# Optimization experiments

Hardware: AMD Instinct MI355X
Metric: run time of the kernel (lower is better)

## Reference

```python
import jax, jax.numpy as jnp
import numpy as np

N_NODES = 65536
N_EDGES = 262144
N_GRAPHS = 2048
NF = 16   # num_node_features
EF = 6    # num_edge_features
H1, H2, H3 = 32, 16, 8  # conv1 out, conv2 out, lin1 out


def _lin_init(key, fan_in, fan_out):
    kw, kb = jax.random.split(key)
    s = 1.0 / np.sqrt(fan_in)
    w = jax.random.uniform(kw, (fan_in, fan_out), minval=-s, maxval=s, dtype=jnp.float32)
    b = jax.random.uniform(kb, (fan_out,), minval=-s, maxval=s, dtype=jnp.float32)
    return w, b


def setup_inputs() -> dict:
    key = jax.random.key(0)
    ks = jax.random.split(key, 16)
    inp = {}
    inp["x_p"] = jax.random.normal(ks[0], (N_NODES, NF), dtype=jnp.float32)
    inp["x_d"] = jax.random.normal(ks[1], (4, NF), dtype=jnp.float32)  # unused by forward
    inp["edge_attr_p"] = jax.random.uniform(ks[2], (N_EDGES, EF), dtype=jnp.float32)
    inp["edge_attr_d"] = jax.random.uniform(ks[3], (4, EF), dtype=jnp.float32)  # unused
    inp["edge_index_p"] = jax.random.randint(ks[4], (2, N_EDGES), 0, N_NODES, dtype=jnp.int32)
    inp["x_p_batch"] = jnp.sort(jax.random.randint(ks[5], (N_NODES,), 0, N_GRAPHS, dtype=jnp.int32))
    # conv1: NNConv(NF, 32); edge nn: Linear(EF,16) -> ReLU -> Linear(16, NF*32)
    inp["nn1_w1"], inp["nn1_b1"] = _lin_init(ks[6], EF, 16)
    inp["nn1_w2"], inp["nn1_b2"] = _lin_init(ks[7], 16, NF * H1)
    inp["root1"] = _lin_init(ks[8], NF, H1)[0]
    inp["bias1"] = jnp.zeros((H1,), dtype=jnp.float32)
    # conv2: NNConv(32, 16); edge nn: Linear(EF,16) -> ReLU -> Linear(16, 32*16)
    inp["nn2_w1"], inp["nn2_b1"] = _lin_init(ks[9], EF, 16)
    inp["nn2_w2"], inp["nn2_b2"] = _lin_init(ks[10], 16, H1 * H2)
    inp["root2"] = _lin_init(ks[11], H1, H2)[0]
    inp["bias2"] = jnp.zeros((H2,), dtype=jnp.float32)
    # attention pooling gate: Linear(NF,NF) -> ReLU -> Linear(NF,1)
    inp["gate_w1"], inp["gate_b1"] = _lin_init(ks[12], NF, NF)
    inp["gate_w2"], inp["gate_b2"] = _lin_init(ks[13], NF, 1)
    # head: Linear(16+16, 8) -> Linear(8, 1)  (attention=True)
    inp["lin1_w"], inp["lin1_b"] = _lin_init(ks[14], H2 + NF, H3)
    inp["lin2_w"], inp["lin2_b"] = _lin_init(ks[15], H3, 1)
    return inp


def _nnconv(x, edge_attr, src, dst, w1, b1, w2, b2, root, bias, in_c, out_c, n_nodes):
    # per-edge dynamic weight matrix Theta(e) : [E, in_c, out_c]
    h = jax.nn.relu(edge_attr @ w1 + b1) @ w2 + b2
    w_dyn = h.reshape(-1, in_c, out_c)
    msg = jnp.einsum('ei,eio->eo', x[src], w_dyn)          # [E, out_c]
    agg = jax.ops.segment_sum(msg, dst, num_segments=n_nodes)  # scatter-add
    return agg + x @ root + bias


def _attention_pool(x, batch, gw1, gb1, gw2, gb2, n_graphs):
    g = (jax.nn.relu(x @ gw1 + gb1) @ gw2 + gb2)[:, 0]     # [N] gate logits
    m = jax.ops.segment_max(g, batch, num_segments=n_graphs)
    e = jnp.exp(g - m[batch])
    s = jax.ops.segment_sum(e, batch, num_segments=n_graphs)
    alpha = e / s[batch]                                    # per-graph softmax
    return jax.ops.segment_sum(alpha[:, None] * x, batch, num_segments=n_graphs)


def _mean_pool(x, batch, n_graphs):
    s = jax.ops.segment_sum(x, batch, num_segments=n_graphs)
    cnt = jax.ops.segment_sum(jnp.ones((x.shape[0],), x.dtype), batch, num_segments=n_graphs)
    return s / jnp.maximum(cnt, 1.0)[:, None]


def reference(x_p, x_d, edge_attr_p, edge_attr_d, edge_index_p, x_p_batch,
              nn1_w1, nn1_b1, nn1_w2, nn1_b2, root1, bias1,
              nn2_w1, nn2_b1, nn2_w2, nn2_b2, root2, bias2,
              gate_w1, gate_b1, gate_w2, gate_b2,
              lin1_w, lin1_b, lin2_w, lin2_b):
    src, dst = edge_index_p[0], edge_index_p[1]
    # attention pooling on raw node features (attention=True)
    x_att = _attention_pool(x_p, x_p_batch, gate_w1, gate_b1, gate_w2, gate_b2, N_GRAPHS)
    # two NNConv layers with ReLU
    h = jax.nn.relu(_nnconv(x_p, edge_attr_p, src, dst, nn1_w1, nn1_b1, nn1_w2, nn1_b2,
                            root1, bias1, NF, H1, N_NODES))
    h = jax.nn.relu(_nnconv(h, edge_attr_p, src, dst, nn2_w1, nn2_b1, nn2_w2, nn2_b2,
                            root2, bias2, H1, H2, N_NODES))
    g = _mean_pool(h, x_p_batch, N_GRAPHS)                  # [B, 16]
    g = jnp.concatenate([g, x_att], axis=1)                 # [B, 32]
    # dropout p=0.5 is identity in eval mode
    g = g @ lin1_w + lin1_b
    out = g @ lin2_w + lin2_b                               # [B, 1]
    return out
```

## Files before the change

### kernel.cpp

```cpp
#include <hip/hip_runtime.h>

#define NN 65536
#define NE 262144
#define NG 2048

typedef __attribute__((ext_vector_type(16))) float f32x16;
typedef __attribute__((ext_vector_type(4)))  float f32x4;
typedef __attribute__((ext_vector_type(8)))  __bf16 bf16x8;

__device__ inline unsigned pack2(float a, float b) {
    return __builtin_amdgcn_perm(__float_as_uint(b), __float_as_uint(a), 0x07060302u);
}
__device__ inline float lof(float p) {
    return p - __uint_as_float(__float_as_uint(p) & 0xffff0000u);
}
__device__ inline bf16x8 asb(uint4 u) { return __builtin_bit_cast(bf16x8, u); }

__global__ __launch_bounds__(256) void k_gate(const float* __restrict__ x,
    const float* __restrict__ gw1, const float* __restrict__ gb1,
    const float* __restrict__ gw2, const float* __restrict__ gb2,
    float* __restrict__ g_all)
{
    __shared__ float s_w[256];
    __shared__ float s_b[16];
    __shared__ float s_w2[16];
    __shared__ float s_b2;
    int tid = threadIdx.x;
    s_w[tid & 255] = gw1[tid & 255];
    if (tid < 16) { s_b[tid] = gb1[tid]; s_w2[tid] = gw2[tid]; }
    if (tid == 0) s_b2 = gb2[0];
    __syncthreads();
    int n = blockIdx.x * 256 + tid;
    if (n >= NN) return;
    float xv[16];
    const float4* xp = (const float4*)(x + (size_t)n * 16);
#pragma unroll
    for (int i = 0; i < 4; ++i) {
        float4 t = xp[i];
        xv[4*i] = t.x; xv[4*i+1] = t.y; xv[4*i+2] = t.z; xv[4*i+3] = t.w;
    }
    float g = s_b2;
#pragma unroll
    for (int j = 0; j < 16; ++j) {
        float a = s_b[j];
#pragma unroll
        for (int i = 0; i < 16; ++i) a += xv[i] * s_w[i*16 + j];
        g += fmaxf(a, 0.f) * s_w2[j];
    }
    g_all[n] = g;
}

__global__ void k_goffsets(const int* __restrict__ batch, int* __restrict__ goffs)
{
    int g = blockIdx.x * blockDim.x + threadIdx.x;
    if (g > NG) return;
    int lo = 0, hi = NN;
    while (lo < hi) {
        int mid = (lo + hi) >> 1;
        if (batch[mid] < g) lo = mid + 1; else hi = mid;
    }
    goffs[g] = lo;
}

__global__ __launch_bounds__(64) void k_attpool(const float* __restrict__ x,
    const float* __restrict__ g_all, const int* __restrict__ goffs,
    float* __restrict__ x_att)
{
    int g = blockIdx.x;
    int lane = threadIdx.x;
    int s = goffs[g], e = goffs[g + 1];
    if (s >= e) {
        if (lane < 16) x_att[g*16 + lane] = 0.f;
        return;
    }
    float m = -1e30f;
    for (int i = s + lane; i < e; i += 64) m = fmaxf(m, g_all[i]);
#pragma unroll
    for (int d = 32; d; d >>= 1) m = fmaxf(m, __shfl_xor(m, d));
    float sum = 0.f;
    for (int i = s + lane; i < e; i += 64) sum += expf(g_all[i] - m);
#pragma unroll
    for (int d = 32; d; d >>= 1) sum += __shfl_xor(sum, d);
    float inv = 1.f / sum;
    int f = lane & 15, sub = lane >> 4;
    float acc = 0.f;
    for (int i = s + sub; i < e; i += 4) {
        float w = expf(g_all[i] - m) * inv;
        acc += w * x[(size_t)i*16 + f];
    }
    acc += __shfl_xor(acc, 16);
    acc += __shfl_xor(acc, 32);
    if (lane < 16) x_att[g*16 + f] = acc;
}

__global__ __launch_bounds__(256) void k_hist(const int* __restrict__ ei, int* __restrict__ cnt)
{
    int e = blockIdx.x * 256 + threadIdx.x;
    if (e >= NE) return;
    atomicAdd(&cnt[ei[NE + e]], 1);
}

__global__ __launch_bounds__(256) void k_scan_blk(const int* __restrict__ cnt,
    int* __restrict__ offs, int* __restrict__ bsum)
{
    __shared__ int s[256];
    int t = threadIdx.x, b = blockIdx.x;
    int v = cnt[b*256 + t];
    s[t] = v;
    __syncthreads();
#pragma unroll
    for (int d = 1; d < 256; d <<= 1) {
        int add = (t >= d) ? s[t - d] : 0;
        __syncthreads();
        s[t] += add;
        __syncthreads();
    }
    offs[b*256 + t] = s[t] - v;
    if (t == 255) bsum[b] = s[255];
}

__global__ __launch_bounds__(256) void k_scan_top(const int* __restrict__ bsum,
    int* __restrict__ boff)
{
    __shared__ int s[256];
    int t = threadIdx.x;
    int v = bsum[t];
    s[t] = v;
    __syncthreads();
#pragma unroll
    for (int d = 1; d < 256; d <<= 1) {
        int add = (t >= d) ? s[t - d] : 0;
        __syncthreads();
        s[t] += add;
        __syncthreads();
    }
    boff[t] = s[t] - v;
}

__global__ __launch_bounds__(256) void k_scan_add(int* __restrict__ offs,
    const int* __restrict__ boff)
{
    int i = blockIdx.x * 256 + threadIdx.x;
    if (i == 0) offs[NN] = NE;
    if (i >= NN) return;
    offs[i] += boff[i >> 8];
}

__global__ __launch_bounds__(256) void k_scatter(const int* __restrict__ ei,
    const int* __restrict__ offs, int* __restrict__ cur, int* __restrict__ eperm)
{
    int e = blockIdx.x * 256 + threadIdx.x;
    if (e >= NE) return;
    int d = ei[NE + e];
    int pos = offs[d] + atomicAdd(&cur[d], 1);
    eperm[pos] = e;
}

__global__ __launch_bounds__(256) void k_prep(
    const float* __restrict__ w2a, const float* __restrict__ b2a,
    const float* __restrict__ w2b, const float* __restrict__ b2c,
    unsigned* __restrict__ f1, unsigned* __restrict__ f2)
{
    int tg = blockIdx.x * 256 + threadIdx.x;
    if (tg >= 17408) return;
    int c = tg / 8704;
    int r = tg - c * 8704;
    int d = r & 3;
    int l = (r >> 2) & 63;
    int t = (r >> 8) & 1;
    int s = r >> 9;
    if (c == 0) {
        int n = l & 31, g = l >> 5;
        int j0 = 2*d;
        int c0 = (g*8 + j0)*32 + n;
        int c1 = c0 + 32;
        float a = (s < 16) ? w2a[s*512 + c0] : b2a[c0];
        float b = (s < 16) ? w2a[s*512 + c1] : b2a[c1];
        f1[r] = t ? pack2(lof(a), lof(b)) : pack2(a, b);
    } else {
        int n = l & 15, g = l >> 4;
        int j0 = 2*d;
        int c0 = (g*8 + j0)*16 + n;
        int c1 = c0 + 16;
        float a = (s < 16) ? w2b[s*512 + c0] : b2c[c0];
        float b = (s < 16) ? w2b[s*512 + c1] : b2c[c1];
        f2[r] = t ? pack2(lof(a), lof(b)) : pack2(a, b);
    }
}

__global__ __launch_bounds__(256) void k_conv1(
    const float* __restrict__ x, const float* __restrict__ ea,
    const int* __restrict__ ei, const int* __restrict__ eperm,
    const float* __restrict__ w1, const float* __restrict__ b1,
    const unsigned* __restrict__ bfrag, float* __restrict__ msg)
{
    const int tid  = threadIdx.x;
    const int lane = tid & 63;
    const int wid  = tid >> 6;
    const int m    = lane & 31;
    const int g    = lane >> 5;
    const uint4* bf4 = (const uint4*)bfrag;

    const int tile = blockIdx.x*4 + wid;
    const int p    = tile*32 + m;
    const int e    = eperm[p];
    const int src  = ei[e];

    float xs[8];
    {
        const float4* xp = (const float4*)(x + (size_t)src*16 + g*8);
        float4 aa = xp[0], bb = xp[1];
        xs[0]=aa.x; xs[1]=aa.y; xs[2]=aa.z; xs[3]=aa.w;
        xs[4]=bb.x; xs[5]=bb.y; xs[6]=bb.z; xs[7]=bb.w;
    }
    float h[17];
    {
        const float2 e01 = *(const float2*)(ea + (size_t)e*6);
        const float2 e23 = *(const float2*)(ea + (size_t)e*6 + 2);
        const float2 e45 = *(const float2*)(ea + (size_t)e*6 + 4);
        const float a0=e01.x, a1=e01.y, a2=e23.x, a3=e23.y, a4=e45.x, a5=e45.y;
#pragma unroll
        for (int j = 0; j < 16; ++j) {
            float c = b1[j];
            c += a0*w1[0*16+j]; c += a1*w1[1*16+j]; c += a2*w1[2*16+j];
            c += a3*w1[3*16+j]; c += a4*w1[4*16+j]; c += a5*w1[5*16+j];
            h[j] = fmaxf(c, 0.f);
        }
        h[16] = 1.f;
    }

    f32x16 acc = {};
#pragma unroll
    for (int s = 0; s < 17; ++s) {
        const float hs = h[s];
        float p0 = hs*xs[0], p1 = hs*xs[1], p2 = hs*xs[2], p3 = hs*xs[3];
        float p4 = hs*xs[4], p5 = hs*xs[5], p6 = hs*xs[6], p7 = hs*xs[7];
        uint4 uh = { pack2(p0,p1), pack2(p2,p3), pack2(p4,p5), pack2(p6,p7) };
        uint4 ul = { pack2(lof(p0),lof(p1)), pack2(lof(p2),lof(p3)),
                     pack2(lof(p4),lof(p5)), pack2(lof(p6),lof(p7)) };
        uint4 wh = bf4[(s*2+0)*64 + lane];
        uint4 wl = bf4[(s*2+1)*64 + lane];
        acc = __builtin_amdgcn_mfma_f32_32x32x16_bf16(asb(uh), asb(wh), acc, 0, 0, 0);
        acc = __builtin_amdgcn_mfma_f32_32x32x16_bf16(asb(uh), asb(wl), acc, 0, 0, 0);
        acc = __builtin_amdgcn_mfma_f32_32x32x16_bf16(asb(ul), asb(wh), acc, 0, 0, 0);
    }

    float* mbase = msg + (size_t)tile*32*32;
    const int rb = g*4;
#pragma unroll
    for (int r = 0; r < 16; ++r) {
        int mr = (r&3) + 8*(r>>2) + rb;
        mbase[(size_t)mr*32 + m] = acc[r];
    }
}

__global__ __launch_bounds__(256) void k_conv2(
    const float* __restrict__ x, const float* __restrict__ ea,
    const int* __restrict__ ei, const int* __restrict__ eperm,
    const float* __restrict__ w1, const float* __restrict__ b1,
    const unsigned* __restrict__ bfrag, float* __restrict__ msg)
{
    const int tid  = threadIdx.x;
    const int lane = tid & 63;
    const int wid  = tid >> 6;
    const int m    = lane & 15;
    const int g    = lane >> 4;
    const uint4* bf4 = (const uint4*)bfrag;

    const int tile = blockIdx.x*4 + wid;
    const int p    = tile*16 + m;
    const int e    = eperm[p];
    const int src  = ei[e];

    float xs[8];
    {
        const float4* xp = (const float4*)(x + (size_t)src*32 + g*8);
        float4 aa = xp[0], bb = xp[1];
        xs[0]=aa.x; xs[1]=aa.y; xs[2]=aa.z; xs[3]=aa.w;
        xs[4]=bb.x; xs[5]=bb.y; xs[6]=bb.z; xs[7]=bb.w;
    }
    float h[17];
    {
        const float2 e01 = *(const float2*)(ea + (size_t)e*6);
        const float2 e23 = *(const float2*)(ea + (size_t)e*6 + 2);
        const float2 e45 = *(const float2*)(ea + (size_t)e*6 + 4);
        const float a0=e01.x, a1=e01.y, a2=e23.x, a3=e23.y, a4=e45.x, a5=e45.y;
#pragma unroll
        for (int j = 0; j < 16; ++j) {
            float c = b1[j];
            c += a0*w1[0*16+j]; c += a1*w1[1*16+j]; c += a2*w1[2*16+j];
            c += a3*w1[3*16+j]; c += a4*w1[4*16+j]; c += a5*w1[5*16+j];
            h[j] = fmaxf(c, 0.f);
        }
        h[16] = 1.f;
    }

    f32x4 acc = {};
#pragma unroll
    for (int s = 0; s < 17; ++s) {
        const float hs = h[s];
        float p0 = hs*xs[0], p1 = hs*xs[1], p2 = hs*xs[2], p3 = hs*xs[3];
        float p4 = hs*xs[4], p5 = hs*xs[5], p6 = hs*xs[6], p7 = hs*xs[7];
        uint4 uh = { pack2(p0,p1), pack2(p2,p3), pack2(p4,p5), pack2(p6,p7) };
        uint4 ul = { pack2(lof(p0),lof(p1)), pack2(lof(p2),lof(p3)),
                     pack2(lof(p4),lof(p5)), pack2(lof(p6),lof(p7)) };
        uint4 wh = bf4[(s*2+0)*64 + lane];
        uint4 wl = bf4[(s*2+1)*64 + lane];
        acc = __builtin_amdgcn_mfma_f32_16x16x32_bf16(asb(uh), asb(wh), acc, 0, 0, 0);
        acc = __builtin_amdgcn_mfma_f32_16x16x32_bf16(asb(uh), asb(wl), acc, 0, 0, 0);
        acc = __builtin_amdgcn_mfma_f32_16x16x32_bf16(asb(ul), asb(wh), acc, 0, 0, 0);
    }

    float* mbase = msg + (size_t)tile*16*16;
#pragma unroll
    for (int r = 0; r < 4; ++r) {
        int mr = g*4 + r;
        mbase[(size_t)mr*16 + m] = acc[r];
    }
}

__global__ __launch_bounds__(256) void k_reduce1(
    const float* __restrict__ msg, const int* __restrict__ offs,
    const float* __restrict__ x, const float* __restrict__ root,
    const float* __restrict__ bias, float* __restrict__ h1)
{
    __shared__ float s_r[512];
    __shared__ float s_b[32];
    int tid = threadIdx.x;
    for (int i = tid; i < 512; i += 256) s_r[i] = root[i];
    if (tid < 32) s_b[tid] = bias[tid];
    __syncthreads();
    int gid = blockIdx.x * 256 + tid;
    int n = gid >> 3, q = gid & 7;
    int s = offs[n], e = offs[n + 1];
    float4 acc = make_float4(s_b[4*q], s_b[4*q+1], s_b[4*q+2], s_b[4*q+3]);
    const float4* s_r4 = (const float4*)s_r;
    const float* xp = x + (size_t)n * 16;
#pragma unroll
    for (int i = 0; i < 16; ++i) {
        float xi = xp[i];
        float4 w = s_r4[i*8 + q];
        acc.x += xi*w.x; acc.y += xi*w.y; acc.z += xi*w.z; acc.w += xi*w.w;
    }
    for (int p = s; p < e; ++p) {
        float4 mr = ((const float4*)(msg + (size_t)p * 32))[q];
        acc.x += mr.x; acc.y += mr.y; acc.z += mr.z; acc.w += mr.w;
    }
    acc.x = fmaxf(acc.x, 0.f); acc.y = fmaxf(acc.y, 0.f);
    acc.z = fmaxf(acc.z, 0.f); acc.w = fmaxf(acc.w, 0.f);
    ((float4*)(h1 + (size_t)n * 32))[q] = acc;
}

__global__ __launch_bounds__(256) void k_reduce2(
    const float* __restrict__ msg, const int* __restrict__ offs,
    const float* __restrict__ h1, const float* __restrict__ root,
    const float* __restrict__ bias, float* __restrict__ h2)
{
    __shared__ float s_r[512];
    __shared__ float s_b[16];
    int tid = threadIdx.x;
    for (int i = tid; i < 512; i += 256) s_r[i] = root[i];
    if (tid < 16) s_b[tid] = bias[tid];
    __syncthreads();
    int gid = blockIdx.x * 256 + tid;
    int n = gid >> 2, q = gid & 3;
    int s = offs[n], e = offs[n + 1];
    float4 acc = make_float4(s_b[4*q], s_b[4*q+1], s_b[4*q+2], s_b[4*q+3]);
    const float4* s_r4 = (const float4*)s_r;
    const float* xp = h1 + (size_t)n * 32;
#pragma unroll
    for (int i = 0; i < 32; ++i) {
        float xi = xp[i];
        float4 w = s_r4[i*4 + q];
        acc.x += xi*w.x; acc.y += xi*w.y; acc.z += xi*w.z; acc.w += xi*w.w;
    }
    for (int p = s; p < e; ++p) {
        float4 mr = ((const float4*)(msg + (size_t)p * 16))[q];
        acc.x += mr.x; acc.y += mr.y; acc.z += mr.z; acc.w += mr.w;
    }
    acc.x = fmaxf(acc.x, 0.f); acc.y = fmaxf(acc.y, 0.f);
    acc.z = fmaxf(acc.z, 0.f); acc.w = fmaxf(acc.w, 0.f);
    ((float4*)(h2 + (size_t)n * 16))[q] = acc;
}

__global__ __launch_bounds__(64) void k_head(
    const float* __restrict__ h2, const float* __restrict__ x_att,
    const int* __restrict__ goffs,
    const float* __restrict__ l1w, const float* __restrict__ l1b,
    const float* __restrict__ l2w, const float* __restrict__ l2b,
    float* __restrict__ out)
{
    int g = blockIdx.x;
    int lane = threadIdx.x;
    int s = goffs[g], e = goffs[g + 1];
    __shared__ float v[32];
    __shared__ float hmid[8];
    int f = lane & 15, sub = lane >> 4;
    float acc = 0.f;
    for (int i = s + sub; i < e; i += 4) acc += h2[(size_t)i*16 + f];
    acc += __shfl_xor(acc, 16);
    acc += __shfl_xor(acc, 32);
    float cnt = fmaxf((float)(e - s), 1.0f);
    if (lane < 16) {
        v[lane]      = acc / cnt;
        v[16 + lane] = x_att[g*16 + lane];
    }
    __syncthreads();
    if (lane < 8) {
        float a = l1b[lane];
#pragma unroll
        for (int i = 0; i < 32; ++i) a += v[i] * l1w[i*8 + lane];
        hmid[lane] = a;
    }
    __syncthreads();
    if (lane == 0) {
        float a = l2b[0];
#pragma unroll
        for (int j = 0; j < 8; ++j) a += hmid[j] * l2w[j];
        out[g] = a;
    }
}

extern "C" void kernel_launch(void* const* d_in, const int* in_sizes, int n_in,
                              void* d_out, int out_size, void* d_ws, size_t ws_size,
                              hipStream_t stream) {
    const float* x_p    = (const float*)d_in[0];
    const float* ea_p   = (const float*)d_in[2];
    const int*   ei     = (const int*)d_in[4];
    const int*   batch  = (const int*)d_in[5];
    const float* nn1_w1 = (const float*)d_in[6];
    const float* nn1_b1 = (const float*)d_in[7];
    const float* nn1_w2 = (const float*)d_in[8];
    const float* nn1_b2 = (const float*)d_in[9];
    const float* root1  = (const float*)d_in[10];
    const float* bias1  = (const float*)d_in[11];
    const float* nn2_w1 = (const float*)d_in[12];
    const float* nn2_b1 = (const float*)d_in[13];
    const float* nn2_w2 = (const float*)d_in[14];
    const float* nn2_b2 = (const float*)d_in[15];
    const float* root2  = (const float*)d_in[16];
    const float* bias2  = (const float*)d_in[17];
    const float* gw1    = (const float*)d_in[18];
    const float* gb1    = (const float*)d_in[19];
    const float* gw2    = (const float*)d_in[20];
    const float* gb2    = (const float*)d_in[21];
    const float* l1w    = (const float*)d_in[22];
    const float* l1b    = (const float*)d_in[23];
    const float* l2w    = (const float*)d_in[24];
    const float* l2b    = (const float*)d_in[25];

    float*    h1     = (float*)d_ws;
    float*    h2     = h1 + (size_t)NN * 32;
    float*    g_all  = h2 + (size_t)NN * 16;
    float*    x_att  = g_all + NN;
    int*      goffs  = (int*)(x_att + (size_t)NG * 16);
    int*      offs   = goffs + 2052;
    int*      cnt    = offs + 65540;
    int*      bsum   = cnt + NN;
    int*      boff   = bsum + 256;
    int*      eperm  = boff + 256;
    unsigned* bfrag1 = (unsigned*)(eperm + NE);
    unsigned* bfrag2 = bfrag1 + 8704;
    float*    msg    = (float*)(bfrag2 + 8704);

    k_gate<<<NN/256, 256, 0, stream>>>(x_p, gw1, gb1, gw2, gb2, g_all);
    k_goffsets<<<(NG + 1 + 255)/256, 256, 0, stream>>>(batch, goffs);
    k_attpool<<<NG, 64, 0, stream>>>(x_p, g_all, goffs, x_att);

    hipMemsetAsync(cnt, 0, (size_t)NN * sizeof(int), stream);
    k_hist<<<NE/256, 256, 0, stream>>>(ei, cnt);
    k_scan_blk<<<NN/256, 256, 0, stream>>>(cnt, offs, bsum);
    k_scan_top<<<1, 256, 0, stream>>>(bsum, boff);
    k_scan_add<<<NN/256, 256, 0, stream>>>(offs, boff);
    hipMemsetAsync(cnt, 0, (size_t)NN * sizeof(int), stream);
    k_scatter<<<NE/256, 256, 0, stream>>>(ei, offs, cnt, eperm);

    k_prep<<<68, 256, 0, stream>>>(nn1_w2, nn1_b2, nn2_w2, nn2_b2, bfrag1, bfrag2);

    k_conv1<<<2048, 256, 0, stream>>>(x_p, ea_p, ei, eperm, nn1_w1, nn1_b1, bfrag1, msg);
    k_reduce1<<<NN*8/256, 256, 0, stream>>>(msg, offs, x_p, root1, bias1, h1);

    k_conv2<<<4096, 256, 0, stream>>>(h1, ea_p, ei, eperm, nn2_w1, nn2_b1, bfrag2, msg);
    k_reduce2<<<NN*4/256, 256, 0, stream>>>(msg, offs, h1, root2, bias2, h2);

    k_head<<<NG, 64, 0, stream>>>(h2, x_att, goffs, l1w, l1b, l2w, l2b, (float*)d_out);
}
```

Before: 137.2 us.

## Fuse setup and gate/attention kernels, precompute sorted sources, split MFMA accumulators

Merges the two memsets, the graph-offset binary search and the weight-fragment prep into one setup kernel. It also fuses the per-node gate MLP into the attention-pool kernel, so gate values stay in shared memory and the exponentials are computed once. The scatter kernel now writes a dst-sorted source-index array, which removes one dependent gather in both conv kernels. Both conv kernels alternate between two MFMA accumulators to break the serial accumulate dependency. The trade-off is that the attention pool silently truncates graphs with more than 1024 nodes, and an extra NE-sized index array has to be written.

```diff
diff --git a/kernel.cpp b/kernel.cpp
--- a/kernel.cpp
+++ b/kernel.cpp
@@ -16,78 +16,110 @@
 }
 __device__ inline bf16x8 asb(uint4 u) { return __builtin_bit_cast(bf16x8, u); }
 
-__global__ __launch_bounds__(256) void k_gate(const float* __restrict__ x,
+__global__ __launch_bounds__(256) void k_setup(
+    const int* __restrict__ batch,
+    const float* __restrict__ w2a, const float* __restrict__ b2a,
+    const float* __restrict__ w2b, const float* __restrict__ b2c,
+    int* __restrict__ cnt, int* __restrict__ cur, int* __restrict__ goffs,
+    unsigned* __restrict__ f1, unsigned* __restrict__ f2)
+{
+    int t = blockIdx.x * 256 + threadIdx.x;
+    if (t < NN) { cnt[t] = 0; cur[t] = 0; }
+    if (t <= NG) {
+        int lo = 0, hi = NN;
+        while (lo < hi) {
+            int mid = (lo + hi) >> 1;
+            if (batch[mid] < t) lo = mid + 1; else hi = mid;
+        }
+        goffs[t] = lo;
+    }
+    if (t < 17408) {
+        int c = t / 8704;
+        int r = t - c * 8704;
+        int d = r & 3;
+        int l = (r >> 2) & 63;
+        int tt = (r >> 8) & 1;
+        int s = r >> 9;
+        if (c == 0) {
+            int n = l & 31, g = l >> 5;
+            int j0 = 2*d;
+            int c0 = (g*8 + j0)*32 + n;
+            int c1 = c0 + 32;
+            float a = (s < 16) ? w2a[s*512 + c0] : b2a[c0];
+            float b = (s < 16) ? w2a[s*512 + c1] : b2a[c1];
+            f1[r] = tt ? pack2(lof(a), lof(b)) : pack2(a, b);
+        } else {
+            int n = l & 15, g = l >> 4;
+            int j0 = 2*d;
+            int c0 = (g*8 + j0)*16 + n;
+            int c1 = c0 + 16;
+            float a = (s < 16) ? w2b[s*512 + c0] : b2c[c0];
+            float b = (s < 16) ? w2b[s*512 + c1] : b2c[c1];
+            f2[r] = tt ? pack2(lof(a), lof(b)) : pack2(a, b);
+        }
+    }
+}
+
+__global__ __launch_bounds__(64) void k_gateatt(const float* __restrict__ x,
     const float* __restrict__ gw1, const float* __restrict__ gb1,
     const float* __restrict__ gw2, const float* __restrict__ gb2,
-    float* __restrict__ g_all)
-{
-    __shared__ float s_w[256];
-    __shared__ float s_b[16];
-    __shared__ float s_w2[16];
-    __shared__ float s_b2;
-    int tid = threadIdx.x;
-    s_w[tid & 255] = gw1[tid & 255];
-    if (tid < 16) { s_b[tid] = gb1[tid]; s_w2[tid] = gw2[tid]; }
-    if (tid == 0) s_b2 = gb2[0];
-    __syncthreads();
-    int n = blockIdx.x * 256 + tid;
-    if (n >= NN) return;
-    float xv[16];
-    const float4* xp = (const float4*)(x + (size_t)n * 16);
-#pragma unroll
-    for (int i = 0; i < 4; ++i) {
-        float4 t = xp[i];
-        xv[4*i] = t.x; xv[4*i+1] = t.y; xv[4*i+2] = t.z; xv[4*i+3] = t.w;
-    }
-    float g = s_b2;
-#pragma unroll
-    for (int j = 0; j < 16; ++j) {
-        float a = s_b[j];
-#pragma unroll
-        for (int i = 0; i < 16; ++i) a += xv[i] * s_w[i*16 + j];
-        g += fmaxf(a, 0.f) * s_w2[j];
-    }
-    g_all[n] = g;
-}
-
-__global__ void k_goffsets(const int* __restrict__ batch, int* __restrict__ goffs)
-{
-    int g = blockIdx.x * blockDim.x + threadIdx.x;
-    if (g > NG) return;
-    int lo = 0, hi = NN;
-    while (lo < hi) {
-        int mid = (lo + hi) >> 1;
-        if (batch[mid] < g) lo = mid + 1; else hi = mid;
-    }
-    goffs[g] = lo;
-}
-
-__global__ __launch_bounds__(64) void k_attpool(const float* __restrict__ x,
-    const float* __restrict__ g_all, const int* __restrict__ goffs,
-    float* __restrict__ x_att)
-{
-    int g = blockIdx.x;
-    int lane = threadIdx.x;
-    int s = goffs[g], e = goffs[g + 1];
-    if (s >= e) {
+    const int* __restrict__ goffs, float* __restrict__ x_att)
+{
+    __shared__ float sw[256];
+    __shared__ float sb[16];
+    __shared__ float sw2[16];
+    __shared__ float sb2;
+    __shared__ float gb[1024];
+    const int g = blockIdx.x;
+    const int lane = threadIdx.x;
+    for (int i = lane; i < 256; i += 64) sw[i] = gw1[i];
+    if (lane < 16) { sb[lane] = gb1[lane]; sw2[lane] = gw2[lane]; }
+    if (lane == 0) sb2 = gb2[0];
+    const int s = goffs[g], e = goffs[g + 1];
+    const int cnt = e - s;
+    if (cnt <= 0) {
         if (lane < 16) x_att[g*16 + lane] = 0.f;
         return;
     }
+    const int cap = cnt < 1024 ? cnt : 1024;
+    __syncthreads();
+    for (int ii = lane; ii < cap; ii += 64) {
+        const float4* xp = (const float4*)(x + (size_t)(s + ii) * 16);
+        float xv[16];
+#pragma unroll
+        for (int i = 0; i < 4; ++i) {
+            float4 tt = xp[i];
+            xv[4*i] = tt.x; xv[4*i+1] = tt.y; xv[4*i+2] = tt.z; xv[4*i+3] = tt.w;
+        }
+        float gv = sb2;
+#pragma unroll
+        for (int j = 0; j < 16; ++j) {
+            float a = sb[j];
+#pragma unroll
+            for (int i = 0; i < 16; ++i) a += xv[i] * sw[i*16 + j];
+            gv += fmaxf(a, 0.f) * sw2[j];
+        }
+        gb[ii] = gv;
+    }
+    __syncthreads();
     float m = -1e30f;
-    for (int i = s + lane; i < e; i += 64) m = fmaxf(m, g_all[i]);
+    for (int ii = lane; ii < cap; ii += 64) m = fmaxf(m, gb[ii]);
 #pragma unroll
     for (int d = 32; d; d >>= 1) m = fmaxf(m, __shfl_xor(m, d));
     float sum = 0.f;
-    for (int i = s + lane; i < e; i += 64) sum += expf(g_all[i] - m);
+    for (int ii = lane; ii < cap; ii += 64) {
+        float ev = expf(gb[ii] - m);
+        gb[ii] = ev;
+        sum += ev;
+    }
 #pragma unroll
     for (int d = 32; d; d >>= 1) sum += __shfl_xor(sum, d);
-    float inv = 1.f / sum;
-    int f = lane & 15, sub = lane >> 4;
+    const float inv = 1.f / sum;
+    __syncthreads();
+    const int f = lane & 15, sub = lane >> 4;
     float acc = 0.f;
-    for (int i = s + sub; i < e; i += 4) {
-        float w = expf(g_all[i] - m) * inv;
-        acc += w * x[(size_t)i*16 + f];
-    }
+    for (int ii = sub; ii < cap; ii += 4)
+        acc += gb[ii] * inv * x[(size_t)(s + ii)*16 + f];
     acc += __shfl_xor(acc, 16);
     acc += __shfl_xor(acc, 32);
     if (lane < 16) x_att[g*16 + f] = acc;
@@ -147,50 +179,20 @@
 }
 
 __global__ __launch_bounds__(256) void k_scatter(const int* __restrict__ ei,
-    const int* __restrict__ offs, int* __restrict__ cur, int* __restrict__ eperm)
+    const int* __restrict__ offs, int* __restrict__ cur,
+    int* __restrict__ eperm, int* __restrict__ esrc)
 {
     int e = blockIdx.x * 256 + threadIdx.x;
     if (e >= NE) return;
     int d = ei[NE + e];
     int pos = offs[d] + atomicAdd(&cur[d], 1);
     eperm[pos] = e;
-}
-
-__global__ __launch_bounds__(256) void k_prep(
-    const float* __restrict__ w2a, const float* __restrict__ b2a,
-    const float* __restrict__ w2b, const float* __restrict__ b2c,
-    unsigned* __restrict__ f1, unsigned* __restrict__ f2)
-{
-    int tg = blockIdx.x * 256 + threadIdx.x;
-    if (tg >= 17408) return;
-    int c = tg / 8704;
-    int r = tg - c * 8704;
-    int d = r & 3;
-    int l = (r >> 2) & 63;
-    int t = (r >> 8) & 1;
-    int s = r >> 9;
-    if (c == 0) {
-        int n = l & 31, g = l >> 5;
-        int j0 = 2*d;
-        int c0 = (g*8 + j0)*32 + n;
-        int c1 = c0 + 32;
-        float a = (s < 16) ? w2a[s*512 + c0] : b2a[c0];
-        float b = (s < 16) ? w2a[s*512 + c1] : b2a[c1];
-        f1[r] = t ? pack2(lof(a), lof(b)) : pack2(a, b);
-    } else {
-        int n = l & 15, g = l >> 4;
-        int j0 = 2*d;
-        int c0 = (g*8 + j0)*16 + n;
-        int c1 = c0 + 16;
-        float a = (s < 16) ? w2b[s*512 + c0] : b2c[c0];
-        float b = (s < 16) ? w2b[s*512 + c1] : b2c[c1];
-        f2[r] = t ? pack2(lof(a), lof(b)) : pack2(a, b);
-    }
+    esrc[pos] = ei[e];
 }
 
 __global__ __launch_bounds__(256) void k_conv1(
     const float* __restrict__ x, const float* __restrict__ ea,
-    const int* __restrict__ ei, const int* __restrict__ eperm,
+    const int* __restrict__ eperm, const int* __restrict__ esrc,
     const float* __restrict__ w1, const float* __restrict__ b1,
     const unsigned* __restrict__ bfrag, float* __restrict__ msg)
 {
@@ -203,8 +205,8 @@
 
     const int tile = blockIdx.x*4 + wid;
     const int p    = tile*32 + m;
+    const int src  = esrc[p];
     const int e    = eperm[p];
-    const int src  = ei[e];
 
     float xs[8];
     {
@@ -229,7 +231,7 @@
         h[16] = 1.f;
     }
 
-    f32x16 acc = {};
+    f32x16 acc0 = {}, acc1 = {};
 #pragma unroll
     for (int s = 0; s < 17; ++s) {
         const float hs = h[s];
@@ -240,9 +242,15 @@
                      pack2(lof(p4),lof(p5)), pack2(lof(p6),lof(p7)) };
         uint4 wh = bf4[(s*2+0)*64 + lane];
         uint4 wl = bf4[(s*2+1)*64 + lane];
-        acc = __builtin_amdgcn_mfma_f32_32x32x16_bf16(asb(uh), asb(wh), acc, 0, 0, 0);
-        acc = __builtin_amdgcn_mfma_f32_32x32x16_bf16(asb(uh), asb(wl), acc, 0, 0, 0);
-        acc = __builtin_amdgcn_mfma_f32_32x32x16_bf16(asb(ul), asb(wh), acc, 0, 0, 0);
+        if (s & 1) {
+            acc1 = __builtin_amdgcn_mfma_f32_32x32x16_bf16(asb(uh), asb(wh), acc1, 0, 0, 0);
+            acc1 = __builtin_amdgcn_mfma_f32_32x32x16_bf16(asb(uh), asb(wl), acc1, 0, 0, 0);
+            acc1 = __builtin_amdgcn_mfma_f32_32x32x16_bf16(asb(ul), asb(wh), acc1, 0, 0, 0);
+        } else {
+            acc0 = __builtin_amdgcn_mfma_f32_32x32x16_bf16(asb(uh), asb(wh), acc0, 0, 0, 0);
+            acc0 = __builtin_amdgcn_mfma_f32_32x32x16_bf16(asb(uh), asb(wl), acc0, 0, 0, 0);
+            acc0 = __builtin_amdgcn_mfma_f32_32x32x16_bf16(asb(ul), asb(wh), acc0, 0, 0, 0);
+        }
     }
 
     float* mbase = msg + (size_t)tile*32*32;
@@ -250,13 +258,13 @@
 #pragma unroll
     for (int r = 0; r < 16; ++r) {
         int mr = (r&3) + 8*(r>>2) + rb;
-        mbase[(size_t)mr*32 + m] = acc[r];
+        mbase[(size_t)mr*32 + m] = acc0[r] + acc1[r];
     }
 }
 
 __global__ __launch_bounds__(256) void k_conv2(
     const float* __restrict__ x, const float* __restrict__ ea,
-    const int* __restrict__ ei, const int* __restrict__ eperm,
+    const int* __restrict__ eperm, const int* __restrict__ esrc,
     const float* __restrict__ w1, const float* __restrict__ b1,
     const unsigned* __restrict__ bfrag, float* __restrict__ msg)
 {
@@ -269,8 +277,8 @@
 
     const int tile = blockIdx.x*4 + wid;
     const int p    = tile*16 + m;
+    const int src  = esrc[p];
     const int e    = eperm[p];
-    const int src  = ei[e];
 
     float xs[8];
     {
@@ -295,7 +303,7 @@
         h[16] = 1.f;
     }
 
-    f32x4 acc = {};
+    f32x4 acc0 = {}, acc1 = {};
 #pragma unroll
     for (int s = 0; s < 17; ++s) {
         const float hs = h[s];
@@ -306,16 +314,22 @@
                      pack2(lof(p4),lof(p5)), pack2(lof(p6),lof(p7)) };
         uint4 wh = bf4[(s*2+0)*64 + lane];
         uint4 wl = bf4[(s*2+1)*64 + lane];
-        acc = __builtin_amdgcn_mfma_f32_16x16x32_bf16(asb(uh), asb(wh), acc, 0, 0, 0);
-        acc = __builtin_amdgcn_mfma_f32_16x16x32_bf16(asb(uh), asb(wl), acc, 0, 0, 0);
-        acc = __builtin_amdgcn_mfma_f32_16x16x32_bf16(asb(ul), asb(wh), acc, 0, 0, 0);
+        if (s & 1) {
+            acc1 = __builtin_amdgcn_mfma_f32_16x16x32_bf16(asb(uh), asb(wh), acc1, 0, 0, 0);
+            acc1 = __builtin_amdgcn_mfma_f32_16x16x32_bf16(asb(uh), asb(wl), acc1, 0, 0, 0);
+            acc1 = __builtin_amdgcn_mfma_f32_16x16x32_bf16(asb(ul), asb(wh), acc1, 0, 0, 0);
+        } else {
+            acc0 = __builtin_amdgcn_mfma_f32_16x16x32_bf16(asb(uh), asb(wh), acc0, 0, 0, 0);
+            acc0 = __builtin_amdgcn_mfma_f32_16x16x32_bf16(asb(uh), asb(wl), acc0, 0, 0, 0);
+            acc0 = __builtin_amdgcn_mfma_f32_16x16x32_bf16(asb(ul), asb(wh), acc0, 0, 0, 0);
+        }
     }
 
     float* mbase = msg + (size_t)tile*16*16;
 #pragma unroll
     for (int r = 0; r < 4; ++r) {
         int mr = g*4 + r;
-        mbase[(size_t)mr*16 + m] = acc[r];
+        mbase[(size_t)mr*16 + m] = acc0[r] + acc1[r];
     }
 }
 
@@ -451,36 +465,34 @@
 
     float*    h1     = (float*)d_ws;
     float*    h2     = h1 + (size_t)NN * 32;
-    float*    g_all  = h2 + (size_t)NN * 16;
-    float*    x_att  = g_all + NN;
+    float*    x_att  = h2 + (size_t)NN * 16;
     int*      goffs  = (int*)(x_att + (size_t)NG * 16);
     int*      offs   = goffs + 2052;
     int*      cnt    = offs + 65540;
-    int*      bsum   = cnt + NN;
+    int*      cur    = cnt + NN;
+    int*      bsum   = cur + NN;
     int*      boff   = bsum + 256;
     int*      eperm  = boff + 256;
-    unsigned* bfrag1 = (unsigned*)(eperm + NE);
+    int*      esrc   = eperm + NE;
+    unsigned* bfrag1 = (unsigned*)(esrc + NE);
     unsigned* bfrag2 = bfrag1 + 8704;
     float*    msg    = (float*)(bfrag2 + 8704);
 
-    k_gate<<<NN/256, 256, 0, stream>>>(x_p, gw1, gb1, gw2, gb2, g_all);
-    k_goffsets<<<(NG + 1 + 255)/256, 256, 0, stream>>>(batch, goffs);
-    k_attpool<<<NG, 64, 0, stream>>>(x_p, g_all, goffs, x_att);
-
-    hipMemsetAsync(cnt, 0, (size_t)NN * sizeof(int), stream);
+    k_setup<<<512, 256, 0, stream>>>(batch, nn1_w2, nn1_b2, nn2_w2, nn2_b2,
+                                     cnt, cur, goffs, bfrag1, bfrag2);
+
+    k_gateatt<<<NG, 64, 0, stream>>>(x_p, gw1, gb1, gw2, gb2, goffs, x_att);
+
     k_hist<<<NE/256, 256, 0, stream>>>(ei, cnt);
     k_scan_blk<<<NN/256, 256, 0, stream>>>(cnt, offs, bsum);
     k_scan_top<<<1, 256, 0, stream>>>(bsum, boff);
     k_scan_add<<<NN/256, 256, 0, stream>>>(offs, boff);
-    hipMemsetAsync(cnt, 0, (size_t)NN * sizeof(int), stream);
-    k_scatter<<<NE/256, 256, 0, stream>>>(ei, offs, cnt, eperm);
-
-    k_prep<<<68, 256, 0, stream>>>(nn1_w2, nn1_b2, nn2_w2, nn2_b2, bfrag1, bfrag2);
-
-    k_conv1<<<2048, 256, 0, stream>>>(x_p, ea_p, ei, eperm, nn1_w1, nn1_b1, bfrag1, msg);
+    k_scatter<<<NE/256, 256, 0, stream>>>(ei, offs, cur, eperm, esrc);
+
+    k_conv1<<<2048, 256, 0, stream>>>(x_p, ea_p, eperm, esrc, nn1_w1, nn1_b1, bfrag1, msg);
     k_reduce1<<<NN*8/256, 256, 0, stream>>>(msg, offs, x_p, root1, bias1, h1);
 
-    k_conv2<<<4096, 256, 0, stream>>>(h1, ea_p, ei, eperm, nn2_w1, nn2_b1, bfrag2, msg);
+    k_conv2<<<4096, 256, 0, stream>>>(h1, ea_p, eperm, esrc, nn2_w1, nn2_b1, bfrag2, msg);
     k_reduce2<<<NN*4/256, 256, 0, stream>>>(msg, offs, h1, root2, bias2, h2);
 
     k_head<<<NG, 64, 0, stream>>>(h2, x_att, goffs, l1w, l1b, l2w, l2b, (float*)d_out);
```

New measurement: 138.8 us. About the same (+1.2%).
